# Optimization experiments

Measured on AMD Instinct MI355X. Metric: run time of the kernel, lower is better.

## Reference

```python
import jax, jax.numpy as jnp
import numpy as np

B = 8192
ID_DIM = 1024
LLM_DIM = 4096
IN_DIM = ID_DIM + LLM_DIM      # 5120
OUT_DIM = 2048
HID = OUT_DIM * 2              # 4096
E = 8
TOPK = 2
GATE_HID = E * 2               # 16


def setup_inputs() -> dict:
    key = jax.random.key(0)
    ks = jax.random.split(key, 12)
    s_in = 1.0 / np.sqrt(IN_DIM)
    s_hid = 1.0 / np.sqrt(HID)
    s_g = 1.0 / np.sqrt(GATE_HID)
    return {
        "id_emb": jax.random.normal(ks[0], (B, ID_DIM), jnp.float32),
        "llm_emb": jax.random.normal(ks[1], (B, LLM_DIM), jnp.float32),
        # stacked expert params
        "W1": jax.random.normal(ks[2], (E, IN_DIM, HID), jnp.float32) * s_in,
        "b1": jax.random.normal(ks[3], (E, HID), jnp.float32) * 0.01,
        "W2": jax.random.normal(ks[4], (E, HID, OUT_DIM), jnp.float32) * s_hid,
        "b2": jax.random.normal(ks[5], (E, OUT_DIM), jnp.float32) * 0.01,
        # gate params
        "gW1": jax.random.normal(ks[6], (IN_DIM, GATE_HID), jnp.float32) * s_in,
        "gb1": jax.random.normal(ks[7], (GATE_HID,), jnp.float32) * 0.01,
        "gW2": jax.random.normal(ks[8], (GATE_HID, E), jnp.float32) * s_g,
        "gb2": jax.random.normal(ks[9], (E,), jnp.float32) * 0.01,
    }


def reference(id_emb, llm_emb, W1, b1, W2, b2, gW1, gb1, gW2, gb2):
    combined = jnp.concatenate([id_emb, llm_emb], axis=-1)          # [B, IN]
    # gate: Linear -> ReLU -> Linear
    gate_logits = jax.nn.relu(combined @ gW1 + gb1) @ gW2 + gb2    # [B, E]
    topk_w, topk_i = jax.lax.top_k(gate_logits, TOPK)               # [B, K]
    topk_w = jax.nn.softmax(topk_w, axis=-1)
    # dense per-expert combine weights [B, E] (zero for non-selected experts)
    bsz = combined.shape[0]
    dense_w = jnp.zeros((bsz, E), combined.dtype).at[
        jnp.arange(bsz)[:, None], topk_i].add(topk_w)
    # dense all-experts MLP (faithful to reference: every expert on all tokens)
    h = jax.nn.relu(jnp.einsum('bi,eih->beh', combined, W1) + b1)  # [B, E, HID]
    expert_out = jnp.einsum('beh,eho->beo', h, W2) + b2            # [B, E, OUT]
    return jnp.einsum('be,beo->bo', dense_w, expert_out)           # [B, OUT]
```

## Files before the change

kernel.cpp:

```cpp
#include <hip/hip_runtime.h>
#include <hip/hip_bf16.h>
#include <hip/hip_fp16.h>

#define B_TOK 8192
#define ID_DIM 1024
#define LLM_DIM 4096
#define IN_DIM 5120
#define OUT_DIM 2048
#define HID 4096
#define NE 8
#define GH 16
#define NSLOT (2 * B_TOK)

#define NNT1 16
#define NKS1 160
#define NNT2 8
#define NKS2 128
#define MT256 72
#define GRID1B (MT256 * NNT1)
#define GRID2B (MT256 * NNT2)

typedef _Float16 f16x8 __attribute__((ext_vector_type(8)));
typedef float f32x4 __attribute__((ext_vector_type(4)));
typedef unsigned short u16;
typedef u16 u16x8 __attribute__((ext_vector_type(8)));

#define OFF_H   (1ull << 20)
#define OFF_X   (OFF_H + (size_t)NSLOT * HID * 2)
#define OFF_P1  (OFF_X + (size_t)B_TOK * IN_DIM * 2)
#define OFF_P2  (OFF_P1 + (size_t)NE * NNT1 * NKS1 * 16384)
#define REQ_WS  (OFF_P2 + (size_t)NE * NNT2 * NKS2 * 16384)
#define OFF_SLOT OFF_P1

#define INV_OFF 66560

__device__ __forceinline__ void gll16(void* lds, const void* gsrc) {
  __builtin_amdgcn_global_load_lds(
      (const __attribute__((address_space(1))) unsigned int*)gsrc,
      (__attribute__((address_space(3))) unsigned int*)lds, 16, 0, 0);
}

__global__ __launch_bounds__(256) void gate_kernel(
    const float* __restrict__ id_emb, const float* __restrict__ llm_emb,
    const float* __restrict__ gW1, const float* __restrict__ gb1,
    const float* __restrict__ gW2, const float* __restrict__ gb2,
    int* __restrict__ wsi, _Float16* __restrict__ xf16) {
  int wave = (blockIdx.x * blockDim.x + threadIdx.x) >> 6;
  int lane = threadIdx.x & 63;
  if (wave >= B_TOK) return;
  int b = wave;
  float acc[GH];
#pragma unroll
  for (int j = 0; j < GH; ++j) acc[j] = 0.f;
  for (int k = lane; k < IN_DIM; k += 64) {
    float x = (k < ID_DIM) ? id_emb[(size_t)b * ID_DIM + k]
                           : llm_emb[(size_t)b * LLM_DIM + (k - ID_DIM)];
    if (xf16) xf16[(size_t)b * IN_DIM + k] = (_Float16)x;
    const float* grow = gW1 + (size_t)k * GH;
#pragma unroll
    for (int j = 0; j < GH; ++j) acc[j] += x * grow[j];
  }
#pragma unroll
  for (int j = 0; j < GH; ++j) {
    for (int off = 32; off > 0; off >>= 1) acc[j] += __shfl_xor(acc[j], off);
  }
  if (lane == 0) {
    float logits[NE];
#pragma unroll
    for (int e = 0; e < NE; ++e) logits[e] = gb2[e];
#pragma unroll
    for (int j = 0; j < GH; ++j) {
      float hg = fmaxf(acc[j] + gb1[j], 0.f);
#pragma unroll
      for (int e = 0; e < NE; ++e) logits[e] += hg * gW2[j * NE + e];
    }
    int i0 = 0; float v0 = logits[0];
#pragma unroll
    for (int e = 1; e < NE; ++e) if (logits[e] > v0) { v0 = logits[e]; i0 = e; }
    int i1 = -1; float v1 = -1e30f;
#pragma unroll
    for (int e = 0; e < NE; ++e) if (e != i0 && logits[e] > v1) { v1 = logits[e]; i1 = e; }
    float ex = expf(v1 - v0);
    float w0 = 1.f / (1.f + ex);
    float w1 = ex / (1.f + ex);
    int* eidx = wsi + 1024;
    float* wsl = (float*)(wsi + 17408);
    eidx[b * 2] = i0; eidx[b * 2 + 1] = i1;
    wsl[b * 2] = w0; wsl[b * 2 + 1] = w1;
    atomicAdd(&wsi[i0], 1);
    atomicAdd(&wsi[i1], 1);
  }
}

__global__ void schedule_kernel(int* __restrict__ wsi) {
  if (threadIdx.x != 0 || blockIdx.x != 0) return;
  int* counts = wsi; int* cursor = wsi + 8;
  int* te = wsi + 16; int* tm = wsi + 272; int* tc = wsi + 528;
  int off = 0, t = 0;
  for (int e = 0; e < NE; ++e) {
    int c = counts[e];
    cursor[e] = off;
    int nt = (c + 255) >> 8;
    for (int i = 0; i < nt; ++i) {
      te[t] = e; tm[t] = off + i * 256;
      int rem = c - i * 256;
      tc[t] = rem < 256 ? rem : 256;
      ++t;
    }
    off += c;
  }
  for (; t < MT256; ++t) { te[t] = 0; tm[t] = 0; tc[t] = 0; }
}

__global__ __launch_bounds__(256) void scatter_kernel(int* __restrict__ wsi) {
  int s = blockIdx.x * blockDim.x + threadIdx.x;
  if (s >= NSLOT) return;
  int* cursor = wsi + 8;
  const int* eidx = wsi + 1024;
  const float* wsl = (const float*)(wsi + 17408);
  int* rows = wsi + 33792;
  float* wsorted = (float*)(wsi + 50176);
  int* inv = wsi + INV_OFF;
  int e = eidx[s];
  int pos = atomicAdd(&cursor[e], 1);
  rows[pos] = s;
  wsorted[pos] = wsl[s];
  inv[s] = pos;
}

__global__ __launch_bounds__(256) void pack_w(
    const float* __restrict__ W, _Float16* __restrict__ P,
    int N, int NNT, int NKS) {
  __shared__ _Float16 lds[32 * 264];
  int ks = blockIdx.x, nt = blockIdx.y, e = blockIdx.z;
  const float* src = W + ((size_t)e * NKS * 32 + (size_t)ks * 32) * N + nt * 256;
  _Float16* dst = P + (((size_t)e * NNT + nt) * NKS + ks) * 8192;
  int t = threadIdx.x;
  int r = t >> 3, c0 = (t & 7) * 32;
  const float* srow = src + (size_t)r * N + c0;
#pragma unroll
  for (int i = 0; i < 4; ++i) {
    float4 v0 = *(const float4*)(srow + i * 8);
    float4 v1 = *(const float4*)(srow + i * 8 + 4);
    union { u16x8 u; _Float16 f[8]; } cv;
    cv.f[0] = (_Float16)v0.x; cv.f[1] = (_Float16)v0.y;
    cv.f[2] = (_Float16)v0.z; cv.f[3] = (_Float16)v0.w;
    cv.f[4] = (_Float16)v1.x; cv.f[5] = (_Float16)v1.y;
    cv.f[6] = (_Float16)v1.z; cv.f[7] = (_Float16)v1.w;
    *(u16x8*)&lds[r * 264 + c0 + i * 8] = cv.u;
  }
  __syncthreads();
  int l = t & 63, q = t >> 6;
  int fr = l & 15, kg = l >> 4;
#pragma unroll
  for (int gi = 0; gi < 4; ++gi) {
    int gn = q * 4 + gi;
    union { u16x8 u; _Float16 f[8]; } cv;
#pragma unroll
    for (int j = 0; j < 8; ++j)
      cv.f[j] = lds[(kg * 8 + j) * 264 + gn * 16 + fr];
    *(u16x8*)(dst + gn * 512 + l * 8) = cv.u;
  }
}

#define SBAR __builtin_amdgcn_s_barrier()
#define SCHB __builtin_amdgcn_sched_barrier(0)
#define VMW(n) asm volatile("s_waitcnt vmcnt(" #n ")" ::: "memory")

#define ST_A(Aw, ks_, pa_, gm_) gll16((Aw) + (gm_) * 512, (pa_) + (size_t)(ks_) * 32)
#define ST_B(Bw, ks_, gn_) \
  gll16((Bw) + (gn_) * 512, pb + (size_t)(ks_) * 8192 + (gn_) * 512)

#define STAGE4(kt)                                                   \
  { _Float16* Aw = smem + ((kt) & 3) * 8192;                         \
    _Float16* Bw = smem + 32768 + ((kt) & 3) * 8192;                 \
    ST_A(Aw, kt, paA, gm_a); ST_A(Aw, kt, paB, gm_b);                \
    ST_B(Bw, kt, gnA); ST_B(Bw, kt, gnB); }

#define READ_A0B(A0s, Bs, Acp, Bcp)                                   \
  _Pragma("unroll") for (int m = 0; m < 4; ++m)                       \
      A0s[m] = *(const f16x8*)((Acp) + (wr * 8 + m) * 512 + lane * 8);\
  _Pragma("unroll") for (int n = 0; n < 4; ++n)                       \
      Bs[n] = *(const f16x8*)((Bcp) + (wc * 4 + n) * 512 + lane * 8);

#define READ_A1(Acp)                                                  \
  _Pragma("unroll") for (int m = 0; m < 4; ++m)                       \
      A1[m] = *(const f16x8*)((Acp) + (wr * 8 + 4 + m) * 512 + lane * 8);

#define MFMA_CL(As, Bs, MO)                                           \
  __builtin_amdgcn_s_setprio(1);                                      \
  _Pragma("unroll") for (int m = 0; m < 4; ++m)                       \
      _Pragma("unroll") for (int n = 0; n < 4; ++n)                   \
          acc[(MO) + m][n] = __builtin_amdgcn_mfma_f32_16x16x32_f16(  \
              As[m], Bs[n], acc[(MO) + m][n], 0, 0, 0);               \
  __builtin_amdgcn_s_setprio(0);

#define PIPE_ITER(A0c, Bc_, A0n, Bn_, k, NKS)                         \
  { if ((k) < (NKS) - 2) { VMW(4); } else { VMW(0); }                 \
    SCHB; SBAR;                                                       \
    if ((k) + 3 < (NKS)) STAGE4((k) + 3);                             \
    _Float16* Acur = smem + ((k) & 3) * 8192;                         \
    READ_A1(Acur); SCHB;                                              \
    MFMA_CL(A0c, Bc_, 0)                                              \
    if ((k) + 1 < (NKS)) {                                            \
      _Float16* An_ = smem + (((k) + 1) & 3) * 8192;                  \
      _Float16* Bn2 = smem + 32768 + (((k) + 1) & 3) * 8192;          \
      READ_A0B(A0n, Bn_, An_, Bn2)                                    \
    }                                                                 \
    SCHB;                                                             \
    MFMA_CL(A1, Bc_, 4) }

#define GEMM_PIPE(NKS)                                                \
  f16x8 A0x[4], Bx[4], A0y[4], By[4], A1[4];                          \
  STAGE4(0) STAGE4(1) STAGE4(2)                                       \
  VMW(8); SCHB; SBAR;                                                 \
  READ_A0B(A0x, Bx, smem, smem + 32768)                               \
  for (int k = 0; k < (NKS); k += 2) {                                \
    PIPE_ITER(A0x, Bx, A0y, By, k, (NKS))                             \
    PIPE_ITER(A0y, By, A0x, Bx, (k + 1), (NKS))                       \
  }

__global__ __launch_bounds__(512, 2) void gemm1_kernel(
    const _Float16* __restrict__ Xf, const _Float16* __restrict__ P1,
    const float* __restrict__ b1, const int* __restrict__ wsi,
    _Float16* __restrict__ hbuf) {
  __shared__ _Float16 smem[65536];
  int d = blockIdx.x;
  int orig = (d & 7) * (GRID1B >> 3) + (d >> 3);
  int tile = orig / NNT1;
  int nt = orig % NNT1;
  int cnt = (wsi + 528)[tile];
  if (cnt == 0) return;
  int e = (wsi + 16)[tile];
  int m0 = (wsi + 272)[tile];
  const int* rows = wsi + 33792;
  int n0 = nt * 256;
  int tid = threadIdx.x, lane = tid & 63, w = tid >> 6;
  int wr = w >> 2, wc = w & 3;
  int fr = lane & 15, kg = lane >> 4;

  int gm_a = wr * 8 + (w & 3);
  int gm_b = gm_a + 4;
  int gnA = w * 2, gnB = w * 2 + 1;
  int ra = gm_a * 16 + fr; ra = ra < cnt ? ra : cnt - 1;
  int rb2 = gm_b * 16 + fr; rb2 = rb2 < cnt ? rb2 : cnt - 1;
  const _Float16* paA = Xf + (size_t)(rows[m0 + ra] >> 1) * IN_DIM + kg * 8;
  const _Float16* paB = Xf + (size_t)(rows[m0 + rb2] >> 1) * IN_DIM + kg * 8;
  const _Float16* pb = P1 + ((size_t)e * NNT1 + nt) * ((size_t)NKS1 * 8192) + lane * 8;

  f32x4 acc[8][4];
#pragma unroll
  for (int m = 0; m < 8; ++m)
#pragma unroll
    for (int n = 0; n < 4; ++n) acc[m][n] = (f32x4){0.f, 0.f, 0.f, 0.f};

  GEMM_PIPE(NKS1)

  float bias_n[4];
#pragma unroll
  for (int n = 0; n < 4; ++n) bias_n[n] = b1[e * HID + n0 + wc * 64 + n * 16 + fr];

  _Float16* ep = smem;
#pragma unroll
  for (int hh = 0; hh < 2; ++hh) {
    __syncthreads();
    if (wr == hh) {
#pragma unroll
      for (int m = 0; m < 8; ++m)
#pragma unroll
        for (int n = 0; n < 4; ++n)
#pragma unroll
          for (int r2 = 0; r2 < 4; ++r2) {
            int row_loc = m * 16 + kg * 4 + r2;
            int col_loc = wc * 64 + n * 16 + fr;
            ep[row_loc * 264 + col_loc] = (_Float16)fmaxf(acc[m][n][r2] + bias_n[n], 0.f);
          }
    }
    __syncthreads();
#pragma unroll
    for (int i = 0; i < 8; ++i) {
      int chunk = i * 512 + tid;
      int row = chunk >> 5, c16 = chunk & 31;
      int r = hh * 128 + row;
      if (r < cnt)
        *(u16x8*)&hbuf[(size_t)(m0 + r) * HID + n0 + c16 * 8] =
            *(const u16x8*)&ep[row * 264 + c16 * 8];
    }
  }
}

__global__ __launch_bounds__(512, 2) void gemm2_kernel(
    const _Float16* __restrict__ hbuf, const _Float16* __restrict__ P2,
    const float* __restrict__ b2, const int* __restrict__ wsi,
    float* __restrict__ slotbuf) {
  __shared__ _Float16 smem[65536];
  int d = blockIdx.x;
  int orig = (d & 7) * (GRID2B >> 3) + (d >> 3);
  int tile = orig / NNT2;
  int nt = orig % NNT2;
  int cnt = (wsi + 528)[tile];
  if (cnt == 0) return;
  int e = (wsi + 16)[tile];
  int m0 = (wsi + 272)[tile];
  const float* wsorted = (const float*)(wsi + 50176);
  int n0 = nt * 256;
  int tid = threadIdx.x, lane = tid & 63, w = tid >> 6;
  int wr = w >> 2, wc = w & 3;
  int fr = lane & 15, kg = lane >> 4;

  int gm_a = wr * 8 + (w & 3);
  int gm_b = gm_a + 4;
  int gnA = w * 2, gnB = w * 2 + 1;
  int ra = gm_a * 16 + fr; ra = ra < cnt ? ra : cnt - 1;
  int rb2 = gm_b * 16 + fr; rb2 = rb2 < cnt ? rb2 : cnt - 1;
  const _Float16* paA = hbuf + (size_t)(m0 + ra) * HID + kg * 8;
  const _Float16* paB = hbuf + (size_t)(m0 + rb2) * HID + kg * 8;
  const _Float16* pb = P2 + ((size_t)e * NNT2 + nt) * ((size_t)NKS2 * 8192) + lane * 8;

  f32x4 acc[8][4];
#pragma unroll
  for (int m = 0; m < 8; ++m)
#pragma unroll
    for (int n = 0; n < 4; ++n) acc[m][n] = (f32x4){0.f, 0.f, 0.f, 0.f};

  GEMM_PIPE(NKS2)

  float bias_n[4];
#pragma unroll
  for (int n = 0; n < 4; ++n) bias_n[n] = b2[e * OUT_DIM + n0 + wc * 64 + n * 16 + fr];

#pragma unroll
  for (int m = 0; m < 8; ++m) {
#pragma unroll
    for (int r2 = 0; r2 < 4; ++r2) {
      int r = wr * 128 + m * 16 + kg * 4 + r2;
      if (r < cnt) {
        float wgt = wsorted[m0 + r];
        float* orow = slotbuf + (size_t)(m0 + r) * OUT_DIM + n0;
#pragma unroll
        for (int n = 0; n < 4; ++n)
          orow[wc * 64 + n * 16 + fr] = (acc[m][n][r2] + bias_n[n]) * wgt;
      }
    }
  }
}

__global__ __launch_bounds__(256) void combine_kernel(
    const float* __restrict__ slotbuf, const int* __restrict__ wsi,
    float* __restrict__ out) {
  int idx = blockIdx.x * 256 + threadIdx.x;
  int b = idx >> 9, c4 = (idx & 511) * 4;
  const int* inv = wsi + INV_OFF;
  int p0 = inv[b * 2], p1 = inv[b * 2 + 1];
  float4 a = *(const float4*)&slotbuf[(size_t)p0 * OUT_DIM + c4];
  float4 c = *(const float4*)&slotbuf[(size_t)p1 * OUT_DIM + c4];
  float4 o; o.x = a.x + c.x; o.y = a.y + c.y; o.z = a.z + c.z; o.w = a.w + c.w;
  *(float4*)&out[(size_t)b * OUT_DIM + c4] = o;
}

#define FB_MAX_TILES 136
__global__ void schedule_fb(int* __restrict__ wsi) {
  if (threadIdx.x != 0 || blockIdx.x != 0) return;
  int* counts = wsi; int* cursor = wsi + 8;
  int* te = wsi + 16; int* tm = wsi + 272; int* tc = wsi + 528;
  int off = 0, t = 0;
  for (int e = 0; e < NE; ++e) {
    int c = counts[e];
    cursor[e] = off;
    int nt = (c + 127) >> 7;
    for (int i = 0; i < nt; ++i) {
      te[t] = e; tm[t] = off + i * 128;
      int rem = c - i * 128;
      tc[t] = rem < 128 ? rem : 128;
      ++t;
    }
    off += c;
  }
  for (; t < FB_MAX_TILES; ++t) { te[t] = 0; tm[t] = 0; tc[t] = 0; }
}

__global__ __launch_bounds__(256, 2) void gemm1_fb(
    const float* __restrict__ id_emb, const float* __restrict__ llm_emb,
    const float* __restrict__ W1, const float* __restrict__ b1,
    const int* __restrict__ wsi, _Float16* __restrict__ h) {
  const int* te = wsi + 16; const int* tm = wsi + 272; const int* tc = wsi + 528;
  const int* rows = wsi + 33792;
  int tile = blockIdx.x;
  int cnt = tc[tile];
  if (cnt == 0) return;
  int e = te[tile], m0 = tm[tile];
  int n0 = blockIdx.y * 128;
  const float* Wb = W1 + (size_t)e * IN_DIM * HID;
  __shared__ _Float16 As[128][40];
  __shared__ _Float16 Bs[128][40];
  int tid = threadIdx.x;
  int lane = tid & 63, w = tid >> 6;
  int wr = w >> 1, wc = w & 1;
  int fr = lane & 15, kg = lane >> 4;
  f32x4 acc[4][4];
#pragma unroll
  for (int m = 0; m < 4; ++m)
#pragma unroll
    for (int n = 0; n < 4; ++n) acc[m][n] = (f32x4){0.f, 0.f, 0.f, 0.f};
  int a_ks = (tid & 3) * 8;
  int a_r = tid >> 2;
  int brow[2];
#pragma unroll
  for (int i = 0; i < 2; ++i) {
    int r = a_r + i * 64;
    brow[i] = (r < cnt) ? (rows[m0 + r] >> 1) : -1;
  }
  int b_c = tid & 127, b_kq = tid >> 7;
  for (int kt = 0; kt < IN_DIM; kt += 32) {
#pragma unroll
    for (int i = 0; i < 2; ++i) {
      int r = a_r + i * 64;
      float v[8];
      if (brow[i] >= 0) {
        int k = kt + a_ks;
        const float* src = (k < ID_DIM)
            ? (id_emb + (size_t)brow[i] * ID_DIM + k)
            : (llm_emb + (size_t)brow[i] * LLM_DIM + (k - ID_DIM));
        float4 v0 = *(const float4*)src;
        float4 v1 = *(const float4*)(src + 4);
        v[0] = v0.x; v[1] = v0.y; v[2] = v0.z; v[3] = v0.w;
        v[4] = v1.x; v[5] = v1.y; v[6] = v1.z; v[7] = v1.w;
      } else {
#pragma unroll
        for (int j = 0; j < 8; ++j) v[j] = 0.f;
      }
      union { u16x8 u; _Float16 f[8]; } cv;
#pragma unroll
      for (int j = 0; j < 8; ++j) cv.f[j] = (_Float16)v[j];
      *reinterpret_cast<u16x8*>(&As[r][a_ks]) = cv.u;
    }
#pragma unroll
    for (int i = 0; i < 2; ++i) {
      int kc = b_kq + i * 2;
      int k0 = kt + kc * 8;
      union { u16x8 u; _Float16 f[8]; } cv;
#pragma unroll
      for (int j = 0; j < 8; ++j)
        cv.f[j] = (_Float16)Wb[(size_t)(k0 + j) * HID + n0 + b_c];
      *reinterpret_cast<u16x8*>(&Bs[b_c][kc * 8]) = cv.u;
    }
    __syncthreads();
    f16x8 af[4], bf[4];
#pragma unroll
    for (int m = 0; m < 4; ++m)
      af[m] = *reinterpret_cast<const f16x8*>(&As[wr * 64 + m * 16 + fr][kg * 8]);
#pragma unroll
    for (int n = 0; n < 4; ++n)
      bf[n] = *reinterpret_cast<const f16x8*>(&Bs[wc * 64 + n * 16 + fr][kg * 8]);
#pragma unroll
    for (int m = 0; m < 4; ++m)
#pragma unroll
      for (int n = 0; n < 4; ++n)
        acc[m][n] = __builtin_amdgcn_mfma_f32_16x16x32_f16(af[m], bf[n], acc[m][n], 0, 0, 0);
    __syncthreads();
  }
#pragma unroll
  for (int m = 0; m < 4; ++m) {
    int rbv = wr * 64 + m * 16 + kg * 4;
#pragma unroll
    for (int n = 0; n < 4; ++n) {
      int col = n0 + wc * 64 + n * 16 + fr;
      float bias = b1[e * HID + col];
#pragma unroll
      for (int r2 = 0; r2 < 4; ++r2) {
        int r = rbv + r2;
        if (r < cnt) {
          float v = fmaxf(acc[m][n][r2] + bias, 0.f);
          h[(size_t)(m0 + r) * HID + col] = (_Float16)v;
        }
      }
    }
  }
}

__global__ __launch_bounds__(256, 2) void gemm2_fb(
    const _Float16* __restrict__ h, const float* __restrict__ W2,
    const float* __restrict__ b2, const int* __restrict__ wsi,
    float* __restrict__ out) {
  const int* te = wsi + 16; const int* tm = wsi + 272; const int* tc = wsi + 528;
  const int* rows = wsi + 33792;
  const float* wsorted = (const float*)(wsi + 50176);
  int tile = blockIdx.x;
  int cnt = tc[tile];
  if (cnt == 0) return;
  int e = te[tile], m0 = tm[tile];
  int n0 = blockIdx.y * 128;
  const float* Wb = W2 + (size_t)e * HID * OUT_DIM;
  __shared__ _Float16 As[128][40];
  __shared__ _Float16 Bs[128][40];
  int tid = threadIdx.x;
  int lane = tid & 63, w = tid >> 6;
  int wr = w >> 1, wc = w & 1;
  int fr = lane & 15, kg = lane >> 4;
  f32x4 acc[4][4];
#pragma unroll
  for (int m = 0; m < 4; ++m)
#pragma unroll
    for (int n = 0; n < 4; ++n) acc[m][n] = (f32x4){0.f, 0.f, 0.f, 0.f};
  int a_ks = (tid & 3) * 8;
  int a_r = tid >> 2;
  int b_c = tid & 127, b_kq = tid >> 7;
  for (int kt = 0; kt < HID; kt += 32) {
#pragma unroll
    for (int i = 0; i < 2; ++i) {
      int r = a_r + i * 64;
      u16x8 v;
      if (r < cnt) {
        v = *reinterpret_cast<const u16x8*>(&h[(size_t)(m0 + r) * HID + kt + a_ks]);
      } else {
        v = (u16x8){0, 0, 0, 0, 0, 0, 0, 0};
      }
      *reinterpret_cast<u16x8*>(&As[r][a_ks]) = v;
    }
#pragma unroll
    for (int i = 0; i < 2; ++i) {
      int kc = b_kq + i * 2;
      int k0 = kt + kc * 8;
      union { u16x8 u; _Float16 f[8]; } cv;
#pragma unroll
      for (int j = 0; j < 8; ++j)
        cv.f[j] = (_Float16)Wb[(size_t)(k0 + j) * OUT_DIM + n0 + b_c];
      *reinterpret_cast<u16x8*>(&Bs[b_c][kc * 8]) = cv.u;
    }
    __syncthreads();
    f16x8 af[4], bf[4];
#pragma unroll
    for (int m = 0; m < 4; ++m)
      af[m] = *reinterpret_cast<const f16x8*>(&As[wr * 64 + m * 16 + fr][kg * 8]);
#pragma unroll
    for (int n = 0; n < 4; ++n)
      bf[n] = *reinterpret_cast<const f16x8*>(&Bs[wc * 64 + n * 16 + fr][kg * 8]);
#pragma unroll
    for (int m = 0; m < 4; ++m)
#pragma unroll
      for (int n = 0; n < 4; ++n)
        acc[m][n] = __builtin_amdgcn_mfma_f32_16x16x32_f16(af[m], bf[n], acc[m][n], 0, 0, 0);
    __syncthreads();
  }
#pragma unroll
  for (int m = 0; m < 4; ++m) {
    int rbv = wr * 64 + m * 16 + kg * 4;
#pragma unroll
    for (int n = 0; n < 4; ++n) {
      int col = n0 + wc * 64 + n * 16 + fr;
      float bias = b2[e * OUT_DIM + col];
#pragma unroll
      for (int r2 = 0; r2 < 4; ++r2) {
        int r = rbv + r2;
        if (r < cnt) {
          int slot = rows[m0 + r];
          int btok = slot >> 1;
          float wgt = wsorted[m0 + r];
          atomicAdd(&out[(size_t)btok * OUT_DIM + col], (acc[m][n][r2] + bias) * wgt);
        }
      }
    }
  }
}

extern "C" void kernel_launch(void* const* d_in, const int* in_sizes, int n_in,
                              void* d_out, int out_size, void* d_ws, size_t ws_size,
                              hipStream_t stream) {
  const float* id_emb  = (const float*)d_in[0];
  const float* llm_emb = (const float*)d_in[1];
  const float* W1  = (const float*)d_in[2];
  const float* b1  = (const float*)d_in[3];
  const float* W2  = (const float*)d_in[4];
  const float* b2  = (const float*)d_in[5];
  const float* gW1 = (const float*)d_in[6];
  const float* gb1 = (const float*)d_in[7];
  const float* gW2 = (const float*)d_in[8];
  const float* gb2 = (const float*)d_in[9];
  float* out = (float*)d_out;
  int* wsi = (int*)d_ws;
  _Float16* h = (_Float16*)((char*)d_ws + OFF_H);
  bool fast = ws_size >= REQ_WS;

  hipMemsetAsync(d_ws, 0, 4096, stream);

  if (fast) {
    _Float16* xf = (_Float16*)((char*)d_ws + OFF_X);
    _Float16* p1 = (_Float16*)((char*)d_ws + OFF_P1);
    _Float16* p2 = (_Float16*)((char*)d_ws + OFF_P2);
    float* slotbuf = (float*)((char*)d_ws + OFF_SLOT);
    gate_kernel<<<B_TOK / 4, 256, 0, stream>>>(id_emb, llm_emb, gW1, gb1, gW2, gb2, wsi, xf);
    schedule_kernel<<<1, 64, 0, stream>>>(wsi);
    scatter_kernel<<<NSLOT / 256, 256, 0, stream>>>(wsi);
    pack_w<<<dim3(NKS1, NNT1, NE), 256, 0, stream>>>(W1, p1, HID, NNT1, NKS1);
    pack_w<<<dim3(NKS2, NNT2, NE), 256, 0, stream>>>(W2, p2, OUT_DIM, NNT2, NKS2);
    gemm1_kernel<<<GRID1B, 512, 0, stream>>>(xf, p1, b1, wsi, h);
    gemm2_kernel<<<GRID2B, 512, 0, stream>>>(h, p2, b2, wsi, slotbuf);
    combine_kernel<<<(B_TOK * OUT_DIM / 4) / 256, 256, 0, stream>>>(slotbuf, wsi, out);
  } else {
    hipMemsetAsync(d_out, 0, (size_t)B_TOK * OUT_DIM * sizeof(float), stream);
    gate_kernel<<<B_TOK / 4, 256, 0, stream>>>(id_emb, llm_emb, gW1, gb1, gW2, gb2, wsi, nullptr);
    schedule_fb<<<1, 64, 0, stream>>>(wsi);
    scatter_kernel<<<NSLOT / 256, 256, 0, stream>>>(wsi);
    gemm1_fb<<<dim3(FB_MAX_TILES, 32), 256, 0, stream>>>(id_emb, llm_emb, W1, b1, wsi, h);
    gemm2_fb<<<dim3(FB_MAX_TILES, 16), 256, 0, stream>>>(h, W2, b2, wsi, out);
  }
}
```

Baseline: 1.854 ms.

## Load B operand directly from global into registers, bypassing LDS staging

The pre-packed weight (B) fragments now go straight from global memory into per-wave registers, one K-step ahead, instead of being staged through LDS. Only the gathered activation (A) tiles stay in the 4-deep LDS ring, which halves shared memory per block and drops the B LDS reads. The epilogue is split into four 64-row passes so it fits the smaller LDS buffer. In exchange, each of the four waves sharing a column group fetches the same B fragments from global/L2 separately, only one step of prefetch hides that latency, and the vmcnt wait counts must match the new mix of outstanding loads.

```diff
diff --git a/kernel.cpp b/kernel.cpp
--- a/kernel.cpp
+++ b/kernel.cpp
@@ -168,22 +168,17 @@
 #define VMW(n) asm volatile("s_waitcnt vmcnt(" #n ")" ::: "memory")
 
 #define ST_A(Aw, ks_, pa_, gm_) gll16((Aw) + (gm_) * 512, (pa_) + (size_t)(ks_) * 32)
-#define ST_B(Bw, ks_, gn_) \
-  gll16((Bw) + (gn_) * 512, pb + (size_t)(ks_) * 8192 + (gn_) * 512)
-
-#define STAGE4(kt)                                                   \
-  { _Float16* Aw = smem + ((kt) & 3) * 8192;                         \
-    _Float16* Bw = smem + 32768 + ((kt) & 3) * 8192;                 \
-    ST_A(Aw, kt, paA, gm_a); ST_A(Aw, kt, paB, gm_b);                \
-    ST_B(Bw, kt, gnA); ST_B(Bw, kt, gnB); }
-
-#define READ_A0B(A0s, Bs, Acp, Bcp)                                   \
+#define STAGE_A(kt)                                                   \
+  { _Float16* Aw = smem + ((kt) & 3) * 8192;                          \
+    ST_A(Aw, kt, paA, gm_a); ST_A(Aw, kt, paB, gm_b); }
+
+#define LOAD_B(Breg, ks_)                                             \
+  _Pragma("unroll") for (int n = 0; n < 4; ++n)                       \
+      Breg[n] = *(const f16x8*)(pbw + (size_t)(ks_) * 8192 + n * 512);
+
+#define READ_A01(Acp)                                                 \
   _Pragma("unroll") for (int m = 0; m < 4; ++m)                       \
-      A0s[m] = *(const f16x8*)((Acp) + (wr * 8 + m) * 512 + lane * 8);\
-  _Pragma("unroll") for (int n = 0; n < 4; ++n)                       \
-      Bs[n] = *(const f16x8*)((Bcp) + (wc * 4 + n) * 512 + lane * 8);
-
-#define READ_A1(Acp)                                                  \
+      A0[m] = *(const f16x8*)((Acp) + (wr * 8 + m) * 512 + lane * 8); \
   _Pragma("unroll") for (int m = 0; m < 4; ++m)                       \
       A1[m] = *(const f16x8*)((Acp) + (wr * 8 + 4 + m) * 512 + lane * 8);
 
@@ -195,36 +190,32 @@
               As[m], Bs[n], acc[(MO) + m][n], 0, 0, 0);               \
   __builtin_amdgcn_s_setprio(0);
 
-#define PIPE_ITER(A0c, Bc_, A0n, Bn_, k, NKS)                         \
-  { if ((k) < (NKS) - 2) { VMW(4); } else { VMW(0); }                 \
+#define PIPE_ITER(Bc_, Bn_, k, NKS)                                   \
+  { if ((k) >= 2 && (k) < (NKS) - 2) { VMW(16); }                     \
+    else if ((k) == 1) { VMW(12); }                                   \
+    else { VMW(8); }                                                  \
     SCHB; SBAR;                                                       \
-    if ((k) + 3 < (NKS)) STAGE4((k) + 3);                             \
+    if ((k) + 3 < (NKS)) STAGE_A((k) + 3);                            \
+    if ((k) + 1 < (NKS)) LOAD_B(Bn_, (k) + 1);                        \
     _Float16* Acur = smem + ((k) & 3) * 8192;                         \
-    READ_A1(Acur); SCHB;                                              \
-    MFMA_CL(A0c, Bc_, 0)                                              \
-    if ((k) + 1 < (NKS)) {                                            \
-      _Float16* An_ = smem + (((k) + 1) & 3) * 8192;                  \
-      _Float16* Bn2 = smem + 32768 + (((k) + 1) & 3) * 8192;          \
-      READ_A0B(A0n, Bn_, An_, Bn2)                                    \
-    }                                                                 \
-    SCHB;                                                             \
+    READ_A01(Acur); SCHB;                                             \
+    MFMA_CL(A0, Bc_, 0)                                               \
     MFMA_CL(A1, Bc_, 4) }
 
 #define GEMM_PIPE(NKS)                                                \
-  f16x8 A0x[4], Bx[4], A0y[4], By[4], A1[4];                          \
-  STAGE4(0) STAGE4(1) STAGE4(2)                                       \
-  VMW(8); SCHB; SBAR;                                                 \
-  READ_A0B(A0x, Bx, smem, smem + 32768)                               \
+  f16x8 A0[4], A1[4], Bx[4], By[4];                                   \
+  STAGE_A(0) STAGE_A(1) STAGE_A(2)                                    \
+  LOAD_B(Bx, 0)                                                       \
   for (int k = 0; k < (NKS); k += 2) {                                \
-    PIPE_ITER(A0x, Bx, A0y, By, k, (NKS))                             \
-    PIPE_ITER(A0y, By, A0x, Bx, (k + 1), (NKS))                       \
+    PIPE_ITER(Bx, By, k, (NKS))                                       \
+    PIPE_ITER(By, Bx, (k + 1), (NKS))                                 \
   }
 
 __global__ __launch_bounds__(512, 2) void gemm1_kernel(
     const _Float16* __restrict__ Xf, const _Float16* __restrict__ P1,
     const float* __restrict__ b1, const int* __restrict__ wsi,
     _Float16* __restrict__ hbuf) {
-  __shared__ _Float16 smem[65536];
+  __shared__ _Float16 smem[32768];
   int d = blockIdx.x;
   int orig = (d & 7) * (GRID1B >> 3) + (d >> 3);
   int tile = orig / NNT1;
@@ -241,12 +232,12 @@
 
   int gm_a = wr * 8 + (w & 3);
   int gm_b = gm_a + 4;
-  int gnA = w * 2, gnB = w * 2 + 1;
   int ra = gm_a * 16 + fr; ra = ra < cnt ? ra : cnt - 1;
   int rb2 = gm_b * 16 + fr; rb2 = rb2 < cnt ? rb2 : cnt - 1;
   const _Float16* paA = Xf + (size_t)(rows[m0 + ra] >> 1) * IN_DIM + kg * 8;
   const _Float16* paB = Xf + (size_t)(rows[m0 + rb2] >> 1) * IN_DIM + kg * 8;
-  const _Float16* pb = P1 + ((size_t)e * NNT1 + nt) * ((size_t)NKS1 * 8192) + lane * 8;
+  const _Float16* pbw = P1 + ((size_t)e * NNT1 + nt) * ((size_t)NKS1 * 8192)
+                         + (size_t)(wc * 4) * 512 + lane * 8;
 
   f32x4 acc[8][4];
 #pragma unroll
@@ -262,26 +253,28 @@
 
   _Float16* ep = smem;
 #pragma unroll
-  for (int hh = 0; hh < 2; ++hh) {
+  for (int q = 0; q < 4; ++q) {
     __syncthreads();
-    if (wr == hh) {
-#pragma unroll
-      for (int m = 0; m < 8; ++m)
+    if (wr == (q >> 1)) {
+#pragma unroll
+      for (int mi = 0; mi < 4; ++mi) {
+        int m = (q & 1) * 4 + mi;
 #pragma unroll
         for (int n = 0; n < 4; ++n)
 #pragma unroll
           for (int r2 = 0; r2 < 4; ++r2) {
-            int row_loc = m * 16 + kg * 4 + r2;
+            int row_loc = mi * 16 + kg * 4 + r2;
             int col_loc = wc * 64 + n * 16 + fr;
             ep[row_loc * 264 + col_loc] = (_Float16)fmaxf(acc[m][n][r2] + bias_n[n], 0.f);
           }
+      }
     }
     __syncthreads();
 #pragma unroll
-    for (int i = 0; i < 8; ++i) {
+    for (int i = 0; i < 4; ++i) {
       int chunk = i * 512 + tid;
       int row = chunk >> 5, c16 = chunk & 31;
-      int r = hh * 128 + row;
+      int r = q * 64 + row;
       if (r < cnt)
         *(u16x8*)&hbuf[(size_t)(m0 + r) * HID + n0 + c16 * 8] =
             *(const u16x8*)&ep[row * 264 + c16 * 8];
@@ -293,7 +286,7 @@
     const _Float16* __restrict__ hbuf, const _Float16* __restrict__ P2,
     const float* __restrict__ b2, const int* __restrict__ wsi,
     float* __restrict__ slotbuf) {
-  __shared__ _Float16 smem[65536];
+  __shared__ _Float16 smem[32768];
   int d = blockIdx.x;
   int orig = (d & 7) * (GRID2B >> 3) + (d >> 3);
   int tile = orig / NNT2;
@@ -310,12 +303,12 @@
 
   int gm_a = wr * 8 + (w & 3);
   int gm_b = gm_a + 4;
-  int gnA = w * 2, gnB = w * 2 + 1;
   int ra = gm_a * 16 + fr; ra = ra < cnt ? ra : cnt - 1;
   int rb2 = gm_b * 16 + fr; rb2 = rb2 < cnt ? rb2 : cnt - 1;
   const _Float16* paA = hbuf + (size_t)(m0 + ra) * HID + kg * 8;
   const _Float16* paB = hbuf + (size_t)(m0 + rb2) * HID + kg * 8;
-  const _Float16* pb = P2 + ((size_t)e * NNT2 + nt) * ((size_t)NKS2 * 8192) + lane * 8;
+  const _Float16* pbw = P2 + ((size_t)e * NNT2 + nt) * ((size_t)NKS2 * 8192)
+                         + (size_t)(wc * 4) * 512 + lane * 8;
 
   f32x4 acc[8][4];
 #pragma unroll
```

New measurement: 2.267 ms. +22.3%, slower.
